# Optimization experiments

Hardware: AMD Instinct MI355X
Metric: run time of the kernel (lower is better)

## Reference

```python
import jax, jax.numpy as jnp
import numpy as np

NUM_HEADS = 8
HEAD_DIM = 64
D_MODEL = NUM_HEADS * HEAD_DIM  # 512
B, T = 4, 2048


def setup_inputs() -> dict:
    key = jax.random.key(0)
    k1, k2 = jax.random.split(key)
    x = jax.random.normal(k1, (B, T, D_MODEL), dtype=jnp.float32)
    mask = jnp.ones((B, 1, T, T), dtype=jnp.float32)
    W = jax.random.normal(k2, (D_MODEL, 3 * D_MODEL), dtype=jnp.float32) * (D_MODEL ** -0.5)
    b = jnp.zeros((3 * D_MODEL,), dtype=jnp.float32)
    return {"x": x, "mask": mask, "W": W, "b": b}


def reference(x, mask, W, b):
    batch = x.shape[0]
    # fused QKV projection: [B, T, 3D]
    qkv = jnp.einsum("btd,de->bte", x, W) + b
    # NOTE: faithful to torch reshape [B, T, H, Hd, 3] -> the size-3 axis is innermost
    qkv = qkv.reshape(batch, -1, NUM_HEADS, HEAD_DIM, 3)
    qkv = jnp.transpose(qkv, (4, 0, 2, 1, 3))  # [3, B, H, T, Hd]
    q, k, v = qkv[0], qkv[1], qkv[2]
    logits = jnp.einsum("bhqd,bhkd->bhqk", q, k) / (HEAD_DIM ** 0.5)
    logits = logits + (1.0 - mask) * -10000.0
    w = jax.nn.softmax(logits, axis=-1)
    out = jnp.einsum("bhqk,bhkd->bhqd", w, v)  # [B, H, T, Hd]
    out = jnp.transpose(out, (0, 2, 1, 3)).reshape(batch, -1, NUM_HEADS * HEAD_DIM)
    return out
```

## Files before the change

kernel.cpp:

```cpp
#include <hip/hip_runtime.h>
#include <hip/hip_bf16.h>
#include <stdint.h>

#define B_   4
#define T_   2048
#define H_   8
#define HD_  64
#define DM_  512
#define N3_  1536

typedef short bf_el;
typedef __attribute__((ext_vector_type(8))) bf_el bfrag;
typedef __attribute__((ext_vector_type(4))) bf_el bhalf4;
typedef __attribute__((ext_vector_type(4))) float ffrag;

#define SCALE_L2E  0.18033688011112043f
#define MASK_L2E   14426.950408889634f

static __device__ __forceinline__ unsigned short f2bf(float f) {
    union { float f; unsigned int i; } v; v.f = f;
    unsigned int r = v.i + 0x7fff + ((v.i >> 16) & 1);
    return (unsigned short)(r >> 16);
}
static __device__ __forceinline__ unsigned short f2bf_fast(float f) {
    union { float f; unsigned int i; } v; v.f = f;
    return (unsigned short)((v.i + 0x8000u) >> 16);
}

static __device__ __forceinline__ unsigned int cvt_pk_bf16(float a, float b) {
    unsigned int r;
    asm("v_cvt_pk_bf16_f32 %0, %1, %2" : "=v"(r) : "v"(a), "v"(b));
    return r;
}

typedef __attribute__((address_space(1))) const unsigned int gu32;
typedef __attribute__((address_space(3))) unsigned int lu32;
static __device__ __forceinline__ void glds16(const unsigned short* g, unsigned short* l) {
    __builtin_amdgcn_global_load_lds((gu32*)g, (lu32*)l, 16, 0, 0);
}

__global__ __launch_bounds__(256) void k_prep(const float* __restrict__ W,
                                              const float* __restrict__ X,
                                              const float* __restrict__ mask,
                                              unsigned short* __restrict__ Wt,
                                              unsigned short* __restrict__ Xb,
                                              int* __restrict__ flags) {
    __shared__ __align__(16) unsigned short Ls[64 * 72];
    const int bid = blockIdx.x;
    const int tid = threadIdx.x;

    if (bid < 512) {
        const int R0 = bid * 16;
        const int mb = R0 >> 11;
        const int q0 = R0 & 2047;
        const int e  = mb * 32 + (q0 >> 6);
        const int wave = tid >> 6, lane = tid & 63;
        unsigned int acc = 0u;
        const float* base = mask + (size_t)R0 * T_ + tid * 8;
#pragma unroll
        for (int rr = 0; rr < 16; ++rr) {
            const uint4 u0 = *(const uint4*)(base + (size_t)rr * T_);
            const uint4 u1 = *(const uint4*)(base + (size_t)rr * T_ + 4);
            acc |= (u0.x ^ 0x3F800000u) | (u0.y ^ 0x3F800000u) |
                   (u0.z ^ 0x3F800000u) | (u0.w ^ 0x3F800000u) |
                   (u1.x ^ 0x3F800000u) | (u1.y ^ 0x3F800000u) |
                   (u1.z ^ 0x3F800000u) | (u1.w ^ 0x3F800000u);
        }
        unsigned long long bal = __ballot(acc != 0u);
        if (lane == 0 && bal != 0ULL) {
            unsigned int bits = 0u;
#pragma unroll
            for (int j = 0; j < 8; ++j)
                if ((bal >> (8 * j)) & 0xFFULL)
                    bits |= (1u << (wave * 8 + j));
            atomicOr((unsigned int*)&flags[e], bits);
        }
        return;
    }
    if (bid < 768) {
        const int b2 = bid - 512;
        const float* src = X + (size_t)b2 * 16384;
        unsigned short* dst = Xb + (size_t)b2 * 16384;
#pragma unroll
        for (int j = 0; j < 8; ++j) {
            int idx = j * 512 + tid * 2;
            float4 f0 = *(const float4*)(src + idx * 4);
            float4 f1 = *(const float4*)(src + idx * 4 + 4);
            __align__(16) unsigned short t8[8];
            t8[0] = f2bf_fast(f0.x); t8[1] = f2bf_fast(f0.y);
            t8[2] = f2bf_fast(f0.z); t8[3] = f2bf_fast(f0.w);
            t8[4] = f2bf_fast(f1.x); t8[5] = f2bf_fast(f1.y);
            t8[6] = f2bf_fast(f1.z); t8[7] = f2bf_fast(f1.w);
            *(uint4*)(dst + idx * 4) = *(const uint4*)t8;
        }
        return;
    }
    {
        const int t  = bid - 768;
        const int n0 = (t % 24) * 64;
        const int k0 = (t / 24) * 64;
#pragma unroll
        for (int i = 0; i < 4; ++i) {
            int chunk = tid + i * 256;
            int k = chunk >> 4;
            int c = chunk & 15;
            float4 f = *(const float4*)(W + (size_t)(k0 + k) * N3_ + n0 + c * 4);
            unsigned short* p = Ls + k * 72 + c * 4;
            p[0] = f2bf(f.x); p[1] = f2bf(f.y); p[2] = f2bf(f.z); p[3] = f2bf(f.w);
        }
        __syncthreads();
        const int n = tid >> 2;
        const int g = tid & 3;
        __align__(16) unsigned short tmp[16];
#pragma unroll
        for (int i = 0; i < 16; ++i) tmp[i] = Ls[(g * 16 + i) * 72 + n];
        uint4* dst = (uint4*)(Wt + (size_t)(n0 + n) * DM_ + k0 + g * 16);
        dst[0] = *(const uint4*)(tmp);
        dst[1] = *(const uint4*)(tmp + 8);
    }
}

__global__ __launch_bounds__(256) void k_gemm_qkv(const unsigned short* __restrict__ Xb,
                                                  const unsigned short* __restrict__ Wt,
                                                  const float* __restrict__ bias,
                                                  unsigned short* __restrict__ Qb,
                                                  unsigned short* __restrict__ Kb,
                                                  unsigned short* __restrict__ Vtb) {
    __shared__ __align__(16) unsigned short SH[12800];
    unsigned short* As = SH;
    unsigned short* Bs = SH + 5120;
    unsigned short* Cs = SH;

    const int tid  = threadIdx.x;
    const int wave = tid >> 6;
    const int lane = tid & 63;
    const int quad = lane >> 4;
    const int l16  = lane & 15;
    const int wm = wave >> 1, wn = wave & 1;
    const int h  = blockIdx.x >> 6;
    const int m0 = (blockIdx.x & 63) * 128;
    const int n0 = h * 192;

    float bvv[6];
#pragma unroll
    for (int ni = 0; ni < 6; ++ni) bvv[ni] = bias[n0 + wn * 96 + ni * 16 + l16];

    ffrag acc[4][6];
#pragma unroll
    for (int i = 0; i < 4; ++i)
#pragma unroll
        for (int j = 0; j < 6; ++j) acc[i][j] = (ffrag){0.f, 0.f, 0.f, 0.f};

    for (int kt = 0; kt < 16; ++kt) {
        __syncthreads();
#pragma unroll
        for (int i = 0; i < 2; ++i) {
            int chunk = tid + i * 256;
            int r = chunk >> 2, c = chunk & 3;
            *(uint4*)(As + r * 40 + c * 8) =
                *(const uint4*)(Xb + (size_t)(m0 + r) * DM_ + kt * 32 + c * 8);
        }
#pragma unroll
        for (int i = 0; i < 3; ++i) {
            int chunk = tid + i * 256;
            int r = chunk >> 2, c = chunk & 3;
            *(uint4*)(Bs + r * 40 + c * 8) =
                *(const uint4*)(Wt + (size_t)(n0 + r) * DM_ + kt * 32 + c * 8);
        }
        __syncthreads();
        bfrag af[4], bfr[6];
#pragma unroll
        for (int mi = 0; mi < 4; ++mi)
            af[mi] = *(const bfrag*)(As + (wm * 64 + mi * 16 + l16) * 40 + quad * 8);
#pragma unroll
        for (int ni = 0; ni < 6; ++ni)
            bfr[ni] = *(const bfrag*)(Bs + (wn * 96 + ni * 16 + l16) * 40 + quad * 8);
#pragma unroll
        for (int mi = 0; mi < 4; ++mi)
#pragma unroll
            for (int ni = 0; ni < 6; ++ni)
                acc[mi][ni] = __builtin_amdgcn_mfma_f32_16x16x32_bf16(af[mi], bfr[ni], acc[mi][ni], 0, 0, 0);
    }

    const int b   = m0 >> 11;
    const int tb0 = m0 & 2047;
    const size_t bh = (size_t)(b * 8 + h);
    float cscale[6];
#pragma unroll
    for (int ni = 0; ni < 6; ++ni) {
        int c = wn * 96 + ni * 16 + l16;
        cscale[ni] = (c % 3 == 0) ? SCALE_L2E : 1.0f;
    }
#pragma unroll
    for (int half = 0; half < 2; ++half) {
        __syncthreads();
        if (wm == half) {
#pragma unroll
            for (int mi = 0; mi < 4; ++mi)
#pragma unroll
                for (int ni = 0; ni < 6; ++ni)
#pragma unroll
                    for (int reg = 0; reg < 4; ++reg) {
                        int r = mi * 16 + quad * 4 + reg;
                        int c = wn * 96 + ni * 16 + l16;
                        Cs[r * 200 + c] = f2bf_fast((acc[mi][ni][reg] + bvv[ni]) * cscale[ni]);
                    }
        }
        __syncthreads();
        const int tb = tb0 + half * 64;
#pragma unroll
        for (int i = 0; i < 2; ++i) {
            int idx = tid + i * 256;
            int tl = idx >> 3, hc = (idx & 7) * 8;
            __align__(16) unsigned short tq[8], tk[8];
#pragma unroll
            for (int j = 0; j < 8; ++j) {
                tq[j] = Cs[tl * 200 + (hc + j) * 3 + 0];
                tk[j] = Cs[tl * 200 + (hc + j) * 3 + 1];
            }
            *(uint4*)(Qb + (bh * T_ + tb + tl) * HD_ + hc) = *(const uint4*)tq;
            *(uint4*)(Kb + (bh * T_ + tb + tl) * HD_ + hc) = *(const uint4*)tk;
        }
#pragma unroll
        for (int i = 0; i < 2; ++i) {
            int idx = tid + i * 256;
            int hd = idx >> 3, t8 = (idx & 7) * 8;
            __align__(16) unsigned short tv[8];
#pragma unroll
            for (int j = 0; j < 8; ++j)
                tv[j] = Cs[(t8 + j) * 200 + hd * 3 + 2];
            *(uint4*)(Vtb + (bh * HD_ + hd) * T_ + tb + t8) = *(const uint4*)tv;
        }
    }
}

__global__ __launch_bounds__(256, 2) void k_attn(const unsigned short* __restrict__ Q,
                                                 const unsigned short* __restrict__ K,
                                                 const unsigned short* __restrict__ Vt,
                                                 const float* __restrict__ mask,
                                                 const int* __restrict__ flags,
                                                 float* __restrict__ out) {
    __shared__ __align__(16) unsigned short SH[17408];
    __shared__ float Rs[256];

    const int tid = threadIdx.x;
    const int wave = tid >> 6, lane = tid & 63;
    const int quad = lane >> 4, l16 = lane & 15;
    const int rg = wave & 1;
    const int kh = wave >> 1;
    const int bh = blockIdx.x & 31, b = bh >> 3, h = bh & 7;
    const int qt = blockIdx.x >> 5;
    const int q0 = qt * 128;

    bfrag qf[4][2];
#pragma unroll
    for (int g = 0; g < 4; ++g) {
        size_t qrow = ((size_t)bh * T_ + q0 + rg * 64 + g * 16 + l16) * HD_;
        qf[g][0] = *(const bfrag*)(Q + qrow + quad * 8);
        qf[g][1] = *(const bfrag*)(Q + qrow + 32 + quad * 8);
    }
    float lsum[4] = {0.f, 0.f, 0.f, 0.f};
    ffrag of[4][4];
#pragma unroll
    for (int g = 0; g < 4; ++g)
#pragma unroll
        for (int nb = 0; nb < 4; ++nb) of[g][nb] = (ffrag){0.f, 0.f, 0.f, 0.f};

    const unsigned int flbits = ((const unsigned int*)flags)[b * 32 + qt * 2 + rg];

    const int lrow = lane >> 3, lcol = lane & 7, swz = lcol ^ lrow;
    const int voffK = lrow * 64 + swz * 8;
    const size_t voffV = (size_t)(wave * 16 + lrow) * T_ + swz * 8;
    const unsigned short* Kbh = K  + (size_t)bh * T_ * HD_;
    const unsigned short* Vbh = Vt + (size_t)bh * HD_ * T_;

    auto STAGE = [&](int buf, int kt) {
        unsigned short* KL = &SH[buf * 4096] + wave * 1024;
        unsigned short* VL = &SH[8192 + buf * 4096] + wave * 1024;
        const unsigned short* kg = Kbh + (size_t)kt * 4096 + wave * 1024 + voffK;
        const unsigned short* vg = Vbh + (size_t)kt * 64 + voffV;
        glds16(kg, KL);
        glds16(kg + 512, KL + 512);
        glds16(vg, VL);
        glds16(vg + (size_t)8 * T_, VL + 512);
    };

    STAGE(0, 0);
    __syncthreads();

    for (int kt = 0; kt < 32; ++kt) {
        const int cur = kt & 1;
        if (kt < 31) STAGE(cur ^ 1, kt + 1);

        const unsigned short* KLc = &SH[cur * 4096];
        const unsigned short* VLc = &SH[8192 + cur * 4096];

        bfrag kf[2][2];
#pragma unroll
        for (int ns = 0; ns < 2; ++ns) {
            const int r = (kh * 2 + ns) * 16 + l16;
#pragma unroll
            for (int ks = 0; ks < 2; ++ks)
                kf[ns][ks] = *(const bfrag*)(KLc + r * 64 + (((ks * 4 + quad) ^ (l16 & 7)) * 8));
        }
        bhalf4 vf[2][4];
#pragma unroll
        for (int nb = 0; nb < 4; ++nb) {
            const int d = nb * 16 + l16;
#pragma unroll
            for (int ns = 0; ns < 2; ++ns)
                vf[ns][nb] = *(const bhalf4*)(VLc + d * 64 +
                                ((kh * 32 + ns * 16 + quad * 4) ^ ((l16 & 7) * 8)));
        }

        const int fl = (int)((flbits >> kt) & 1u);
#pragma unroll
        for (int g = 0; g < 4; ++g) {
            ffrag st[2];
#pragma unroll
            for (int ns = 0; ns < 2; ++ns) {
                ffrag a = (ffrag){0.f, 0.f, 0.f, 0.f};
                a = __builtin_amdgcn_mfma_f32_16x16x32_bf16(kf[ns][0], qf[g][0], a, 0, 0, 0);
                a = __builtin_amdgcn_mfma_f32_16x16x32_bf16(kf[ns][1], qf[g][1], a, 0, 0, 0);
                st[ns] = a;
            }
            float p[2][4];
            if (fl) {
                const float* mrow = mask + ((size_t)b * T_ + q0 + rg * 64 + g * 16 + l16) * T_
                                  + kt * 64 + kh * 32 + quad * 4;
#pragma unroll
                for (int ns = 0; ns < 2; ++ns) {
                    float mv[4];
                    *(float4*)mv = *(const float4*)(mrow + ns * 16);
#pragma unroll
                    for (int reg = 0; reg < 4; ++reg) {
                        float pv = __builtin_amdgcn_exp2f(
                            fmaf(mv[reg], MASK_L2E, st[ns][reg] - MASK_L2E));
                        p[ns][reg] = pv;
                        lsum[g] += pv;
                    }
                }
            } else {
#pragma unroll
                for (int ns = 0; ns < 2; ++ns)
#pragma unroll
                    for (int reg = 0; reg < 4; ++reg) {
                        float pv = __builtin_amdgcn_exp2f(st[ns][reg]);
                        p[ns][reg] = pv;
                        lsum[g] += pv;
                    }
            }
            union { unsigned int u[4]; bfrag s; } pa;
            pa.u[0] = cvt_pk_bf16(p[0][0], p[0][1]);
            pa.u[1] = cvt_pk_bf16(p[0][2], p[0][3]);
            pa.u[2] = cvt_pk_bf16(p[1][0], p[1][1]);
            pa.u[3] = cvt_pk_bf16(p[1][2], p[1][3]);
#pragma unroll
            for (int nb = 0; nb < 4; ++nb) {
                union { bhalf4 h[2]; bfrag f; } vv;
                vv.h[0] = vf[0][nb];
                vv.h[1] = vf[1][nb];
                of[g][nb] = __builtin_amdgcn_mfma_f32_16x16x32_bf16(pa.s, vv.f, of[g][nb], 0, 0, 0);
            }
        }
        if (kt < 31) __syncthreads();
    }

    float rsw[4];
#pragma unroll
    for (int g = 0; g < 4; ++g) {
        float r = lsum[g];
        r += __shfl_xor(r, 16, 64);
        r += __shfl_xor(r, 32, 64);
        rsw[g] = r;
    }
    __syncthreads();
    float* Fp = (float*)SH;
    if (quad == 0) {
#pragma unroll
        for (int g = 0; g < 4; ++g)
            Rs[kh * 128 + rg * 64 + g * 16 + l16] = rsw[g];
    }
    if (kh == 1) {
        float* basep = Fp + rg * (64 * 66);
#pragma unroll
        for (int g = 0; g < 4; ++g)
#pragma unroll
            for (int nb = 0; nb < 4; ++nb)
#pragma unroll
                for (int reg = 0; reg < 4; ++reg)
                    basep[(g * 16 + quad * 4 + reg) * 66 + nb * 16 + l16] = of[g][nb][reg];
    }
    __syncthreads();
    if (kh == 0) {
        const float* basep = Fp + rg * (64 * 66);
#pragma unroll
        for (int g = 0; g < 4; ++g) {
            float inv[4];
#pragma unroll
            for (int reg = 0; reg < 4; ++reg) {
                int row = rg * 64 + g * 16 + quad * 4 + reg;
                inv[reg] = 1.0f / (Rs[row] + Rs[128 + row]);
            }
#pragma unroll
            for (int nb = 0; nb < 4; ++nb)
#pragma unroll
                for (int reg = 0; reg < 4; ++reg) {
                    float v = of[g][nb][reg] + basep[(g * 16 + quad * 4 + reg) * 66 + nb * 16 + l16];
                    int t = q0 + rg * 64 + g * 16 + quad * 4 + reg;
                    out[((size_t)b * T_ + t) * DM_ + h * 64 + nb * 16 + l16] = v * inv[reg];
                }
        }
    }
}

extern "C" void kernel_launch(void* const* d_in, const int* in_sizes, int n_in,
                              void* d_out, int out_size, void* d_ws, size_t ws_size,
                              hipStream_t stream) {
    const float* X    = (const float*)d_in[0];
    const float* mask = (const float*)d_in[1];
    const float* W    = (const float*)d_in[2];
    const float* bias = (const float*)d_in[3];
    float* outp = (float*)d_out;

    char* ws = (char*)d_ws;
    unsigned short* Wt  = (unsigned short*)(ws);
    unsigned short* Xb  = (unsigned short*)(ws + 1572864);
    unsigned short* Qb  = (unsigned short*)(ws + 9961472);
    unsigned short* Kb  = (unsigned short*)(ws + 18350080);
    unsigned short* Vtb = (unsigned short*)(ws + 26738688);
    int*            flg = (int*)(ws + 35127296);

    hipMemsetAsync(flg, 0, 512, stream);
    k_prep     <<<dim3(960), 256, 0, stream>>>(W, X, mask, Wt, Xb, flg);
    k_gemm_qkv <<<dim3(512), 256, 0, stream>>>(Xb, Wt, bias, Qb, Kb, Vtb);
    k_attn     <<<dim3(512), 256, 0, stream>>>(Qb, Kb, Vtb, mask, flg, outp);
}
```

Baseline: 199.7 us.

## Deepen K/V LDS pipeline to four stages and compute row sums via MFMA

Expands the shared K/V staging from double to quadruple buffering with prefetch distance two, replacing the per-iteration __syncthreads with explicit vmcnt waits plus a single s_barrier. Row-sum accumulation of softmax weights moves from scalar VALU adds and cross-lane shuffles to an extra MFMA against a ones vector, and s_setprio brackets the MFMA sections. This targets load latency stalls and VALU pressure, at the cost of doubled LDS (which may limit occupancy to fewer blocks per CU) and extra accumulator registers.

```diff
diff --git a/kernel.cpp b/kernel.cpp
--- a/kernel.cpp
+++ b/kernel.cpp
@@ -38,6 +38,9 @@
 static __device__ __forceinline__ void glds16(const unsigned short* g, unsigned short* l) {
     __builtin_amdgcn_global_load_lds((gu32*)g, (lu32*)l, 16, 0, 0);
 }
+
+#define VMCNT(n) do { asm volatile("s_waitcnt vmcnt(" #n ")" ::: "memory"); \
+                      __builtin_amdgcn_sched_barrier(0); } while (0)
 
 __global__ __launch_bounds__(256) void k_prep(const float* __restrict__ W,
                                               const float* __restrict__ X,
@@ -240,7 +243,7 @@
                                                  const float* __restrict__ mask,
                                                  const int* __restrict__ flags,
                                                  float* __restrict__ out) {
-    __shared__ __align__(16) unsigned short SH[17408];
+    __shared__ __align__(16) unsigned short SH[32768];
     __shared__ float Rs[256];
 
     const int tid = threadIdx.x;
@@ -259,12 +262,15 @@
         qf[g][0] = *(const bfrag*)(Q + qrow + quad * 8);
         qf[g][1] = *(const bfrag*)(Q + qrow + 32 + quad * 8);
     }
-    float lsum[4] = {0.f, 0.f, 0.f, 0.f};
-    ffrag of[4][4];
+    ffrag of[4][5];
 #pragma unroll
     for (int g = 0; g < 4; ++g)
 #pragma unroll
-        for (int nb = 0; nb < 4; ++nb) of[g][nb] = (ffrag){0.f, 0.f, 0.f, 0.f};
+        for (int nb = 0; nb < 5; ++nb) of[g][nb] = (ffrag){0.f, 0.f, 0.f, 0.f};
+
+    bfrag vones;
+#pragma unroll
+    for (int j = 0; j < 8; ++j) vones[j] = (short)0x3F80;
 
     const unsigned int flbits = ((const unsigned int*)flags)[b * 32 + qt * 2 + rg];
 
@@ -276,7 +282,7 @@
 
     auto STAGE = [&](int buf, int kt) {
         unsigned short* KL = &SH[buf * 4096] + wave * 1024;
-        unsigned short* VL = &SH[8192 + buf * 4096] + wave * 1024;
+        unsigned short* VL = &SH[16384 + buf * 4096] + wave * 1024;
         const unsigned short* kg = Kbh + (size_t)kt * 4096 + wave * 1024 + voffK;
         const unsigned short* vg = Vbh + (size_t)kt * 64 + voffV;
         glds16(kg, KL);
@@ -286,14 +292,18 @@
     };
 
     STAGE(0, 0);
-    __syncthreads();
+    STAGE(1, 1);
 
     for (int kt = 0; kt < 32; ++kt) {
-        const int cur = kt & 1;
-        if (kt < 31) STAGE(cur ^ 1, kt + 1);
-
+        if (kt < 30) STAGE((kt + 2) & 3, kt + 2);
+        if (kt < 30)      { VMCNT(8); }
+        else if (kt == 30){ VMCNT(4); }
+        else              { VMCNT(0); }
+        __builtin_amdgcn_s_barrier();
+
+        const int cur = kt & 3;
         const unsigned short* KLc = &SH[cur * 4096];
-        const unsigned short* VLc = &SH[8192 + cur * 4096];
+        const unsigned short* VLc = &SH[16384 + cur * 4096];
 
         bfrag kf[2][2];
 #pragma unroll
@@ -317,6 +327,7 @@
 #pragma unroll
         for (int g = 0; g < 4; ++g) {
             ffrag st[2];
+            __builtin_amdgcn_s_setprio(1);
 #pragma unroll
             for (int ns = 0; ns < 2; ++ns) {
                 ffrag a = (ffrag){0.f, 0.f, 0.f, 0.f};
@@ -324,6 +335,7 @@
                 a = __builtin_amdgcn_mfma_f32_16x16x32_bf16(kf[ns][1], qf[g][1], a, 0, 0, 0);
                 st[ns] = a;
             }
+            __builtin_amdgcn_s_setprio(0);
             float p[2][4];
             if (fl) {
                 const float* mrow = mask + ((size_t)b * T_ + q0 + rg * 64 + g * 16 + l16) * T_
@@ -333,28 +345,23 @@
                     float mv[4];
                     *(float4*)mv = *(const float4*)(mrow + ns * 16);
 #pragma unroll
-                    for (int reg = 0; reg < 4; ++reg) {
-                        float pv = __builtin_amdgcn_exp2f(
+                    for (int reg = 0; reg < 4; ++reg)
+                        p[ns][reg] = __builtin_amdgcn_exp2f(
                             fmaf(mv[reg], MASK_L2E, st[ns][reg] - MASK_L2E));
-                        p[ns][reg] = pv;
-                        lsum[g] += pv;
-                    }
                 }
             } else {
 #pragma unroll
                 for (int ns = 0; ns < 2; ++ns)
 #pragma unroll
-                    for (int reg = 0; reg < 4; ++reg) {
-                        float pv = __builtin_amdgcn_exp2f(st[ns][reg]);
-                        p[ns][reg] = pv;
-                        lsum[g] += pv;
-                    }
+                    for (int reg = 0; reg < 4; ++reg)
+                        p[ns][reg] = __builtin_amdgcn_exp2f(st[ns][reg]);
             }
             union { unsigned int u[4]; bfrag s; } pa;
             pa.u[0] = cvt_pk_bf16(p[0][0], p[0][1]);
             pa.u[1] = cvt_pk_bf16(p[0][2], p[0][3]);
             pa.u[2] = cvt_pk_bf16(p[1][0], p[1][1]);
             pa.u[3] = cvt_pk_bf16(p[1][2], p[1][3]);
+            __builtin_amdgcn_s_setprio(1);
 #pragma unroll
             for (int nb = 0; nb < 4; ++nb) {
                 union { bhalf4 h[2]; bfrag f; } vv;
@@ -362,24 +369,19 @@
                 vv.h[1] = vf[1][nb];
                 of[g][nb] = __builtin_amdgcn_mfma_f32_16x16x32_bf16(pa.s, vv.f, of[g][nb], 0, 0, 0);
             }
-        }
-        if (kt < 31) __syncthreads();
-    }
-
-    float rsw[4];
-#pragma unroll
-    for (int g = 0; g < 4; ++g) {
-        float r = lsum[g];
-        r += __shfl_xor(r, 16, 64);
-        r += __shfl_xor(r, 32, 64);
-        rsw[g] = r;
-    }
+            of[g][4] = __builtin_amdgcn_mfma_f32_16x16x32_bf16(pa.s, vones, of[g][4], 0, 0, 0);
+            __builtin_amdgcn_s_setprio(0);
+        }
+    }
+
     __syncthreads();
     float* Fp = (float*)SH;
-    if (quad == 0) {
+    if (l16 == 0) {
 #pragma unroll
         for (int g = 0; g < 4; ++g)
-            Rs[kh * 128 + rg * 64 + g * 16 + l16] = rsw[g];
+#pragma unroll
+            for (int reg = 0; reg < 4; ++reg)
+                Rs[kh * 128 + rg * 64 + g * 16 + quad * 4 + reg] = of[g][4][reg];
     }
     if (kh == 1) {
         float* basep = Fp + rg * (64 * 66);
```

After: 196.3 us. Within noise of the previous version (-1.7%).
